# Kernel optimization log

Hardware: AMD Instinct MI355X
Metric: run time of the kernel (lower is better)

## Reference

```python
import jax, jax.numpy as jnp
import numpy as np

N_NODES = 10000
N_EDGES = 160000


def _conv2d(x, w, b):
    y = jax.lax.conv_general_dilated(x, w, (1, 1), 'SAME',
                                     dimension_numbers=('NCHW', 'OIHW', 'NCHW'))
    return jax.nn.selu(y + b[None, :, None, None])


def _cnn(cf, cnn_w1, cnn_b1, cnn_w2, cnn_b2, cnn_w3, cnn_b3, cnn_w4, cnn_b4):
    h = _conv2d(cf, cnn_w1, cnn_b1)
    h = _conv2d(h, cnn_w2, cnn_b2)
    h = _conv2d(h, cnn_w3, cnn_b3)
    h = _conv2d(h, cnn_w4, cnn_b4)
    return h.mean(axis=(2, 3))  # (1, 24) global avg pool


def _gat(x, src, dst, W, a_s, a_d, b, n):
    # PyG GATConv, concat=False (mean over heads), add_self_loops handled by caller
    H, C = a_s.shape
    h = (x @ W).reshape(-1, H, C)                      # (N,H,C)
    e = jax.nn.leaky_relu((h * a_s).sum(-1)[src] +
                          (h * a_d).sum(-1)[dst], 0.2)  # (E,H)
    m = jax.ops.segment_max(e, dst, num_segments=n)
    p = jnp.exp(e - m[dst])
    z = jax.ops.segment_sum(p, dst, num_segments=n)
    alpha = p / (z[dst] + 1e-16)
    out = jax.ops.segment_sum(h[src] * alpha[..., None], dst, num_segments=n)
    return out.mean(axis=1) + b


def _fix_boundary(v, up, down, left, right):
    c0 = jnp.where(down, 0.0, jnp.where(up, 1.0, v[:, 0]))
    c1 = jnp.where(right, 1.0, jnp.where(left, 0.0, v[:, 1]))
    return v.at[:, 0].set(c0).at[:, 1].set(c1)


def setup_inputs() -> dict:
    key = jax.random.key(0)
    ks = jax.random.split(key, 40)
    d = {}
    d['x'] = jax.random.uniform(ks[0], (N_NODES, 10), dtype=jnp.float32)
    d['edge_index'] = jax.random.randint(ks[1], (2, N_EDGES), 0, N_NODES, dtype=jnp.int64)
    d['conv_feat'] = jax.random.normal(ks[2], (1, 4, 64, 64), dtype=jnp.float32)
    cnn_dims = [(16, 4), (32, 16), (64, 32), (24, 64)]
    for i, (o, c) in enumerate(cnn_dims, 1):
        d[f'cnn_w{i}'] = jax.random.normal(ks[2 + i], (o, c, 3, 3), jnp.float32) * 0.1
        d[f'cnn_b{i}'] = jnp.zeros((o,), jnp.float32)
    gat_dims = [(34, 8, 64), (64, 16, 128), (128, 8, 256), (256, 8, 128), (128, 16, 2)]
    for i, (fin, H, C) in enumerate(gat_dims, 1):
        k1, k2, k3 = jax.random.split(ks[10 + i], 3)
        d[f'g{i}_w'] = jax.random.normal(k1, (fin, H * C), jnp.float32) * 0.1
        d[f'g{i}_as'] = jax.random.normal(k2, (H, C), jnp.float32) * 0.1
        d[f'g{i}_ad'] = jax.random.normal(k3, (H, C), jnp.float32) * 0.1
        d[f'g{i}_b'] = jnp.zeros((C,), jnp.float32)
    return d


def reference(x, edge_index, conv_feat,
              cnn_w1, cnn_b1, cnn_w2, cnn_b2, cnn_w3, cnn_b3, cnn_w4, cnn_b4,
              g1_w, g1_as, g1_ad, g1_b,
              g2_w, g2_as, g2_ad, g2_b,
              g3_w, g3_as, g3_ad, g3_b,
              g4_w, g4_as, g4_ad, g4_b,
              g5_w, g5_as, g5_ad, g5_b):
    n = x.shape[0]
    # boundary masks from raw node coordinates
    up, down = x[:, 0] == 1, x[:, 0] == 0
    left, right = x[:, 1] == 0, x[:, 1] == 1
    # add self loops (PyG GATConv default)
    loops = jnp.arange(n, dtype=edge_index.dtype)
    src = jnp.concatenate([edge_index[0], loops])
    dst = jnp.concatenate([edge_index[1], loops])

    gfeat = _cnn(conv_feat, cnn_w1, cnn_b1, cnn_w2, cnn_b2, cnn_w3, cnn_b3, cnn_w4, cnn_b4)
    h = jnp.concatenate([jnp.broadcast_to(gfeat, (n, gfeat.shape[1])), x], axis=1)

    h = jax.nn.selu(_gat(h, src, dst, g1_w, g1_as, g1_ad, g1_b, n))
    h = _fix_boundary(h, up, down, left, right)
    h = jax.nn.selu(_gat(h, src, dst, g2_w, g2_as, g2_ad, g2_b, n))
    h = _fix_boundary(h, up, down, left, right)
    h = jax.nn.selu(_gat(h, src, dst, g3_w, g3_as, g3_ad, g3_b, n))
    h = _fix_boundary(h, up, down, left, right)
    h = jax.nn.selu(_gat(h, src, dst, g4_w, g4_as, g4_ad, g4_b, n))
    h = _fix_boundary(h, up, down, left, right)
    res = jax.nn.selu(_gat(h, src, dst, g5_w, g5_as, g5_ad, g5_b, n))
    out = x[:, :2] + res
    out = _fix_boundary(out, up, down, left, right)
    return out
```

## Files before the change

kernel.cpp:

```cpp
#include <hip/hip_runtime.h>
#include <hip/hip_fp16.h>
#include <math.h>


#define DEVFN static __device__ __forceinline__

typedef __attribute__((ext_vector_type(8))) _Float16 half8;
typedef __attribute__((ext_vector_type(4))) _Float16 half4v;
typedef __attribute__((ext_vector_type(4))) float f32x4;

DEVFN float selu_f(float v) {
    const float scale = 1.0507009873554805f;
    const float alpha = 1.6732632423543772f;
    return v > 0.f ? scale * v : scale * alpha * (expf(v) - 1.f);
}

DEVFN float lrelu02(float v) { return v > 0.f ? v : 0.2f * v; }

#define PST 66
#define PSZ (66 * 66)

__global__ __launch_bounds__(256) void conv3x3_first(const float* __restrict__ cf,
                                                     const float* __restrict__ w,
                                                     const float* __restrict__ b,
                                                     float* __restrict__ out) {
    int x  = threadIdx.x & 63;
    int yg = threadIdx.x >> 6;
    int y  = blockIdx.x * 4 + yg;
    int co = blockIdx.y;
    float acc = b[co];
    const float* wp = w + (size_t)co * 4 * 9;
#pragma unroll
    for (int ci = 0; ci < 4; ++ci) {
        const float* ip = cf + ci * 4096;
        const float* wr = wp + ci * 9;
#pragma unroll
        for (int ky = 0; ky < 3; ++ky) {
            int yy = y + ky - 1;
            if (yy < 0 || yy >= 64) continue;
#pragma unroll
            for (int kx = 0; kx < 3; ++kx) {
                int xx = x + kx - 1;
                if (xx < 0 || xx >= 64) continue;
                acc += wr[ky * 3 + kx] * ip[yy * 64 + xx];
            }
        }
    }
    out[(size_t)co * PSZ + (y + 1) * PST + (x + 1)] = selu_f(acc);
}

template <int CIN>
__global__ __launch_bounds__(256) void conv3x3_pad(const float* __restrict__ in,
                                                   const float* __restrict__ w,
                                                   const float* __restrict__ b,
                                                   float* __restrict__ out) {
    int x  = threadIdx.x & 63;
    int yg = threadIdx.x >> 6;
    int y  = blockIdx.x * 4 + yg;
    int co = blockIdx.y;
    float acc = b[co];
    const float* wp = w + (size_t)co * CIN * 9;
#pragma unroll 4
    for (int ci = 0; ci < CIN; ++ci) {
        const float* ip = in + ci * PSZ + y * PST + x;
        const float* wr = wp + ci * 9;
        acc += wr[0] * ip[0]           + wr[1] * ip[1]           + wr[2] * ip[2]
             + wr[3] * ip[PST]         + wr[4] * ip[PST + 1]     + wr[5] * ip[PST + 2]
             + wr[6] * ip[2 * PST]     + wr[7] * ip[2 * PST + 1] + wr[8] * ip[2 * PST + 2];
    }
    out[(size_t)co * PSZ + (y + 1) * PST + (x + 1)] = selu_f(acc);
}

__global__ void avgpool_c(const float* __restrict__ in, float* __restrict__ gfeat) {
    int c = blockIdx.x;
    int t = threadIdx.x;
    float s = 0.f;
    for (int i = t; i < 4096; i += 256) {
        int y = i >> 6, x = i & 63;
        s += in[c * PSZ + (y + 1) * PST + (x + 1)];
    }
#pragma unroll
    for (int off = 32; off >= 1; off >>= 1) s += __shfl_xor(s, off);
    __shared__ float red[4];
    int wave = t >> 6, lane = t & 63;
    if (lane == 0) red[wave] = s;
    __syncthreads();
    if (t == 0) gfeat[c] = (red[0] + red[1] + red[2] + red[3]) * (1.f / 4096.f);
}

__global__ void build_h0(const float* __restrict__ x, const float* __restrict__ gfeat,
                         __half* __restrict__ h0f, unsigned* __restrict__ masks, int N) {
    int n = blockIdx.x * blockDim.x + threadIdx.x;
    if (n >= N) return;
    float x0 = x[n * 10 + 0], x1 = x[n * 10 + 1];
    unsigned mk = (x0 == 1.f ? 1u : 0u) | (x0 == 0.f ? 2u : 0u) |
                  (x1 == 0.f ? 4u : 0u) | (x1 == 1.f ? 8u : 0u);
    masks[n] = mk;
    __half* hq = h0f + (size_t)n * 64;
#pragma unroll
    for (int j = 0; j < 64; ++j) {
        float v = (j < 24) ? gfeat[j] : (j < 34 ? x[n * 10 + (j - 24)] : 0.f);
        hq[j] = __float2half(v);
    }
}

__global__ void count_dst(const int* __restrict__ ei, int* __restrict__ cnt, int E, int N) {
    int t = blockIdx.x * blockDim.x + threadIdx.x;
    if (t >= E + N) return;
    int dst = (t < E) ? ei[E + t] : (t - E);
    atomicAdd(&cnt[dst], 1);
}

__global__ __launch_bounds__(1024) void scan_all(const int* __restrict__ cnt,
                                                 int* __restrict__ indptr,
                                                 int* __restrict__ cursor,
                                                 int n, int total) {
    __shared__ int sdata[1024];
    int t = threadIdx.x;
    int base = t * 10;
    int loc[10];
    int s = 0;
#pragma unroll
    for (int i = 0; i < 10; ++i) {
        int idx = base + i;
        int v = (idx < n) ? cnt[idx] : 0;
        loc[i] = s;
        s += v;
    }
    sdata[t] = s;
    __syncthreads();
    for (int off = 1; off < 1024; off <<= 1) {
        int tmp = (t >= off) ? sdata[t - off] : 0;
        __syncthreads();
        sdata[t] += tmp;
        __syncthreads();
    }
    int excl = (t == 0) ? 0 : sdata[t - 1];
#pragma unroll
    for (int i = 0; i < 10; ++i) {
        int idx = base + i;
        if (idx < n) {
            int e = excl + loc[i];
            indptr[idx] = e;
            cursor[idx] = e;
        }
    }
    if (t == 0) indptr[n] = total;
}

__global__ void scatter_edges(const int* __restrict__ ei, int* __restrict__ cursor,
                              int* __restrict__ col, int E, int N) {
    int t = blockIdx.x * blockDim.x + threadIdx.x;
    if (t >= E + N) return;
    int src, dst;
    if (t < E) { src = ei[t]; dst = ei[E + t]; }
    else       { src = dst = t - E; }
    int pos = atomicAdd(&cursor[dst], 1);
    col[pos] = src;
}

__global__ __launch_bounds__(256) void prep_all(
        const float* __restrict__ W0, const float* __restrict__ W1,
        const float* __restrict__ W2, const float* __restrict__ W3,
        const float* __restrict__ W4,
        const float* __restrict__ as0, const float* __restrict__ as1,
        const float* __restrict__ as2, const float* __restrict__ as3,
        const float* __restrict__ as4,
        const float* __restrict__ ad0, const float* __restrict__ ad1,
        const float* __restrict__ ad2, const float* __restrict__ ad3,
        const float* __restrict__ ad4,
        unsigned short* __restrict__ bt, float* __restrict__ wesed,
        float* __restrict__ wcomb) {
    const int Kc[5]  = {34, 64, 128, 256, 128};
    const int Kpc[5] = {64, 64, 128, 256, 128};
    const int Hc[5]  = {8, 16, 8, 8, 16};
    const int Cc[5]  = {64, 128, 256, 128, 2};
    const int HCc[5] = {512, 2048, 2048, 1024, 32};
    const int KAc[5] = {512, 1024, 1024, 2048, 2048};
    const int btOff[5] = {0, 32768, 163840, 425984, 0};
    const int weOff[5] = {0, 1024, 3072, 5120, 9216};

    int b = blockIdx.x, tid = threadIdx.x;

    if (b < 168) {
        int lyr, tloc;
        if (b < 8)        { lyr = 0; tloc = b; }
        else if (b < 40)  { lyr = 1; tloc = b - 8; }
        else if (b < 104) { lyr = 2; tloc = b - 40; }
        else              { lyr = 3; tloc = b - 104; }
        const int ktl[4] = {1, 1, 2, 4};
        const int mtl[4] = {1, 2, 4, 2};
        int kt = ktl[lyr], mt = mtl[lyr];
        int per_h = kt * mt;
        int h = tloc / per_h, r = tloc - h * per_h;
        int ki = r % kt, mi = r / kt;
        int k0 = ki * 64, m0 = mi * 64;
        int K = Kc[lyr], Kp = Kpc[lyr], C = Cc[lyr], HC = HCc[lyr], KA = KAc[lyr];
        const float* W;
        if (lyr == 0) W = W0; else if (lyr == 1) W = W1;
        else if (lyr == 2) W = W2; else W = W3;

        __shared__ float tile[64][65];
        int c = tid & 63, rg = tid >> 6;
        for (int r2 = rg; r2 < 64; r2 += 4) {
            int k = k0 + r2, m = m0 + c;
            float v = (k < K && m < C) ? W[(size_t)k * HC + h * C + m] : 0.f;
            tile[r2][c] = v;
        }
        __syncthreads();
        unsigned short* bp = bt + btOff[lyr];
        for (int mr = rg; mr < 64; mr += 4) {
            int m = m0 + mr, k = k0 + c;
            if (m < C && k < Kp)
                bp[(size_t)m * KA + h * Kp + k] =
                    __half_as_ushort(__float2half(tile[c][mr]));
        }
    } else if (b < 200) {
        int u = (b - 168) * 256 + tid;
        int k = u >> 6, o = u & 63;
        float s;
        if (o < 32) {
            int h = (o < 16) ? o : o - 16;
            const float* av = ((o < 16) ? as4 : ad4) + h * 2;
            s = W4[k * 32 + h * 2 + 0] * av[0] + W4[k * 32 + h * 2 + 1] * av[1];
        } else {
            s = W4[k * 32 + (o - 32)];
        }
        wcomb[u] = s;
    } else {
        int wb = b - 200;
        int lyr, u0;
        if (wb < 4)       { lyr = 0; u0 = wb * 256; }
        else if (wb < 12) { lyr = 1; u0 = (wb - 4) * 256; }
        else if (wb < 20) { lyr = 2; u0 = (wb - 12) * 256; }
        else if (wb < 36) { lyr = 3; u0 = (wb - 20) * 256; }
        else              { lyr = 4; u0 = (wb - 36) * 256; }
        int u = u0 + tid;
        int K = Kc[lyr], Kp = Kpc[lyr], H = Hc[lyr], C = Cc[lyr], HC = HCc[lyr];
        int H2 = 2 * H;
        if (u < Kp * H2) {
            int k = u / H2, o = u - k * H2;
            float s = 0.f;
            if (k < K) {
                int h = (o < H) ? o : o - H;
                const float *W, *as_, *ad_;
                if (lyr == 0)      { W = W0; as_ = as0; ad_ = ad0; }
                else if (lyr == 1) { W = W1; as_ = as1; ad_ = ad1; }
                else if (lyr == 2) { W = W2; as_ = as2; ad_ = ad2; }
                else if (lyr == 3) { W = W3; as_ = as3; ad_ = ad3; }
                else               { W = W4; as_ = as4; ad_ = ad4; }
                const float* av = ((o < H) ? as_ : ad_) + h * C;
                const float* wp = W + (size_t)k * HC + h * C;
#pragma unroll 4
                for (int c2 = 0; c2 < C; ++c2) s += wp[c2] * av[c2];
            }
            wesed[weOff[lyr] + u] = s;
        }
    }
}

__global__ void esed_kernel(const __half* __restrict__ hin, const float* __restrict__ wesed,
                            float* __restrict__ esed, int N, int Kp, int H2) {
    int t = blockIdx.x * blockDim.x + threadIdx.x;
    if (t >= N * H2) return;
    int n = t / H2, o = t - n * H2;
    const __half2* hp = (const __half2*)(hin + (size_t)n * Kp);
    float s = 0.f;
    for (int k2 = 0; k2 < Kp / 2; ++k2) {
        float2 f = __half22float2(hp[k2]);
        s += f.x * wesed[(2 * k2) * H2 + o] + f.y * wesed[(2 * k2 + 1) * H2 + o];
    }
    esed[t] = s;
}

template <int H, int KP, int CH, int NPB>
__global__ __launch_bounds__(NPB * (KP / CH)) void gat_fused_lds(
        const __half* __restrict__ hinf, const float* __restrict__ esed,
        const int* __restrict__ indptr, const int* __restrict__ col,
        __half* __restrict__ g, int N) {
    const int TPN = KP / CH;
    const int EC  = TPN / H;
    const int H2  = 2 * H;
    __shared__ float lds_p[NPB][2][TPN];
    int sub = threadIdx.x / TPN;
    int j   = threadIdx.x % TPN;
    int n = blockIdx.x * NPB + sub;
    if (n >= N) return;
    int e_my = j / H, h_my = j % H;
    int c0 = j * CH;
    float edv = esed[n * H2 + H + h_my];

    float acc[H][CH];
#pragma unroll
    for (int h = 0; h < H; ++h)
#pragma unroll
        for (int t = 0; t < CH; ++t) acc[h][t] = 0.f;
    float zloc = 0.f;

    int beg = indptr[n], deg = indptr[n + 1] - beg;

    float p = 0.f;
    if (e_my < deg) {
        int srcm = col[beg + e_my];
        p = expf(lrelu02(esed[srcm * H2 + h_my] + edv));
    }
    int buf = 0;
    for (int base = 0; base < deg; base += EC) {
        zloc += p;
        lds_p[sub][buf][j] = p;
        __builtin_amdgcn_wave_barrier();
        int ce = base + EC + e_my;
        bool vnext = (ce < deg);
        float esv = 0.f;
        if (vnext) {
            int srcm = col[beg + ce];
            esv = esed[srcm * H2 + h_my];
        }
#pragma unroll
        for (int e = 0; e < EC; ++e) {
            int idx = base + e;
            if (idx < deg) {
                int src = col[beg + idx];
                float f[CH];
                if (CH == 2) {
                    __half2 hv = *(const __half2*)(hinf + (size_t)src * KP + c0);
                    float2 ff = __half22float2(hv);
                    f[0] = ff.x; f[1] = ff.y;
                } else {
                    half4v hv = *(const half4v*)(hinf + (size_t)src * KP + c0);
                    f[0] = (float)hv[0]; f[1] = (float)hv[1];
                    f[2] = (float)hv[2]; f[3] = (float)hv[3];
                }
                const float4* ap = (const float4*)&lds_p[sub][buf][e * H];
#pragma unroll
                for (int q4 = 0; q4 < H / 4; ++q4) {
                    float4 a4 = ap[q4];
#pragma unroll
                    for (int t = 0; t < CH; ++t) {
                        acc[4 * q4 + 0][t] += a4.x * f[t];
                        acc[4 * q4 + 1][t] += a4.y * f[t];
                        acc[4 * q4 + 2][t] += a4.z * f[t];
                        acc[4 * q4 + 3][t] += a4.w * f[t];
                    }
                }
            }
        }
        p = vnext ? expf(lrelu02(esv + edv)) : 0.f;
        buf ^= 1;
    }

#pragma unroll
    for (int off = H; off < TPN; off <<= 1)
        zloc += __shfl_xor(zloc, off, TPN);
    float zinv_my = (1.f / H) / (zloc + 1e-16f);

    __half* gp = g + (size_t)n * (H * KP) + c0;
#pragma unroll
    for (int h = 0; h < H; ++h) {
        float zf = __shfl(zinv_my, h, TPN);
        if (CH == 2) {
            *(__half2*)(gp + h * KP) =
                __floats2half2_rn(acc[h][0] * zf, acc[h][1] * zf);
        } else {
            __half2 lo = __floats2half2_rn(acc[h][0] * zf, acc[h][1] * zf);
            __half2 hi = __floats2half2_rn(acc[h][2] * zf, acc[h][3] * zf);
            union { __half2 h2[2]; float2 f2; } u;
            u.h2[0] = lo; u.h2[1] = hi;
            *(float2*)(gp + h * KP) = u.f2;
        }
    }
}

template <int NPB>
__global__ __launch_bounds__(NPB * 32) void final_attn(
        const float* __restrict__ eyp, const int* __restrict__ indptr,
        const int* __restrict__ col, const float* __restrict__ b5,
        const unsigned* __restrict__ masks, const float* __restrict__ x,
        float* __restrict__ outp, int N) {
    int sub = threadIdx.x >> 5;
    int j   = threadIdx.x & 31;
    int n = blockIdx.x * NPB + sub;
    if (n >= N) return;
    int h = j >> 1;
    float edv = eyp[(size_t)n * 64 + 16 + h];
    int beg = indptr[n], end = indptr[n + 1];
    float z = 0.f, a = 0.f;
    int i = beg;
    for (; i + 1 < end; i += 2) {
        int s0 = col[i], s1 = col[i + 1];
        const float* r0 = eyp + (size_t)s0 * 64;
        const float* r1 = eyp + (size_t)s1 * 64;
        float es0 = r0[h], y0 = r0[32 + j];
        float es1 = r1[h], y1 = r1[32 + j];
        float p0 = expf(lrelu02(es0 + edv));
        float p1 = expf(lrelu02(es1 + edv));
        z += p0; a += p0 * y0;
        z += p1; a += p1 * y1;
    }
    for (; i < end; ++i) {
        const float* r = eyp + (size_t)col[i] * 64;
        float p = expf(lrelu02(r[h] + edv));
        z += p; a += p * r[32 + j];
    }
    float zf = (1.f / 16.f) / (z + 1e-16f);
    float val = a * zf;
#pragma unroll
    for (int off = 2; off <= 16; off <<= 1) val += __shfl_xor(val, off, 32);
    float other = __shfl_xor(val, 1, 32);
    if (j == 0) {
        unsigned mk = masks[n];
        float v0 = x[n * 10 + 0] + selu_f(val + b5[0]);
        float v1 = x[n * 10 + 1] + selu_f(other + b5[1]);
        if (mk & 2u) v0 = 0.f; else if (mk & 1u) v0 = 1.f;
        if (mk & 8u) v1 = 1.f; else if (mk & 4u) v1 = 0.f;
        outp[n * 2 + 0] = v0;
        outp[n * 2 + 1] = v1;
    }
}

#define LDP 72

__global__ __launch_bounds__(256) void gemm_lds(const __half* __restrict__ A,
                                                const unsigned short* __restrict__ Bhi,
                                                const float* __restrict__ bias,
                                                const unsigned* __restrict__ masks,
                                                __half* __restrict__ O16,
                                                int N, int K, int M) {
    __shared__ __half lA[64 * LDP], lB[64 * LDP];
    int tid = threadIdx.x;
    int wave = tid >> 6, lane = tid & 63;
    int ln16 = lane & 15, q = lane >> 4;
    int row0 = blockIdx.x * 64;
    int col0 = blockIdx.y * 64;

    int r0 = tid >> 3, r1 = r0 + 32;
    int ac = (tid & 7) * 8;
    int ga0 = min(row0 + r0, N - 1);
    int ga1 = min(row0 + r1, N - 1);
    const __half* Bp = (const __half*)Bhi;
    const __half* a0p = A + (size_t)ga0 * K + ac;
    const __half* a1p = A + (size_t)ga1 * K + ac;
    const __half* b0p = Bp + (size_t)(col0 + r0) * K + ac;
    const __half* b1p = Bp + (size_t)(col0 + r1) * K + ac;

    half8 ra0 = *(const half8*)(a0p);
    half8 ra1 = *(const half8*)(a1p);
    half8 rb0 = *(const half8*)(b0p);
    half8 rb1 = *(const half8*)(b1p);

    f32x4 acc[4];
#pragma unroll
    for (int j = 0; j < 4; ++j) acc[j] = (f32x4){0.f, 0.f, 0.f, 0.f};

    for (int kc = 0; kc < K; kc += 64) {
        __syncthreads();
        *(half8*)(lA + r0 * LDP + ac) = ra0;
        *(half8*)(lA + r1 * LDP + ac) = ra1;
        *(half8*)(lB + r0 * LDP + ac) = rb0;
        *(half8*)(lB + r1 * LDP + ac) = rb1;
        __syncthreads();
        int kn = kc + 64;
        if (kn < K) {
            ra0 = *(const half8*)(a0p + kn);
            ra1 = *(const half8*)(a1p + kn);
            rb0 = *(const half8*)(b0p + kn);
            rb1 = *(const half8*)(b1p + kn);
        }
#pragma unroll
        for (int kk = 0; kk < 2; ++kk) {
            half8 af = *(const half8*)(lA + (wave * 16 + ln16) * LDP + kk * 32 + q * 8);
#pragma unroll
            for (int j = 0; j < 4; ++j) {
                half8 bf = *(const half8*)(lB + (j * 16 + ln16) * LDP + kk * 32 + q * 8);
                acc[j] = __builtin_amdgcn_mfma_f32_16x16x32_f16(af, bf, acc[j], 0, 0, 0);
            }
        }
    }

#pragma unroll
    for (int j = 0; j < 4; ++j) {
        int cc = col0 + j * 16 + ln16;
        float bv = bias[cc];
#pragma unroll
        for (int r = 0; r < 4; ++r) {
            int rr = row0 + wave * 16 + q * 4 + r;
            if (rr >= N) continue;
            float v = selu_f(acc[j][r] + bv);
            if (cc < 2) {
                unsigned mk = masks[rr];
                if (cc == 0) { if (mk & 2u) v = 0.f; else if (mk & 1u) v = 1.f; }
                else         { if (mk & 8u) v = 1.f; else if (mk & 4u) v = 0.f; }
            }
            O16[(size_t)rr * M + cc] = __float2half(v);
        }
    }
}

__global__ __launch_bounds__(256) void gemm_rc(const __half* __restrict__ A,
                                               const unsigned short* __restrict__ Bhi,
                                               const float* __restrict__ bias,
                                               const unsigned* __restrict__ masks,
                                               __half* __restrict__ O16,
                                               int N, int K, int M) {
    __shared__ __half lA[32 * LDP], lB[128 * LDP];
    int tid = threadIdx.x;
    int wave = tid >> 6, lane = tid & 63;
    int ln16 = lane & 15, q = lane >> 4;
    int row0 = blockIdx.x * 32;
    int col0 = blockIdx.y * 128;
    int wr = (wave >> 1) * 16;
    int wc = (wave & 1) * 64;

    int ar = tid >> 3;
    int ac = (tid & 7) * 8;
    int ga = min(row0 + ar, N - 1);
    const __half* ap  = A + (size_t)ga * K + ac;
    const __half* Bp  = (const __half*)Bhi;
    const __half* b0p = Bp + (size_t)(col0 + ar) * K + ac;
    const __half* b1p = Bp + (size_t)(col0 + ar + 32) * K + ac;
    const __half* b2p = Bp + (size_t)(col0 + ar + 64) * K + ac;
    const __half* b3p = Bp + (size_t)(col0 + ar + 96) * K + ac;

    half8 ra  = *(const half8*)(ap);
    half8 rb0 = *(const half8*)(b0p);
    half8 rb1 = *(const half8*)(b1p);
    half8 rb2 = *(const half8*)(b2p);
    half8 rb3 = *(const half8*)(b3p);

    f32x4 acc[4];
#pragma unroll
    for (int j = 0; j < 4; ++j) acc[j] = (f32x4){0.f, 0.f, 0.f, 0.f};

    for (int kc = 0; kc < K; kc += 64) {
        __syncthreads();
        *(half8*)(lA + ar * LDP + ac)        = ra;
        *(half8*)(lB + ar * LDP + ac)        = rb0;
        *(half8*)(lB + (ar + 32) * LDP + ac) = rb1;
        *(half8*)(lB + (ar + 64) * LDP + ac) = rb2;
        *(half8*)(lB + (ar + 96) * LDP + ac) = rb3;
        __syncthreads();
        int kn = kc + 64;
        if (kn < K) {
            ra  = *(const half8*)(ap + kn);
            rb0 = *(const half8*)(b0p + kn);
            rb1 = *(const half8*)(b1p + kn);
            rb2 = *(const half8*)(b2p + kn);
            rb3 = *(const half8*)(b3p + kn);
        }
#pragma unroll
        for (int kk = 0; kk < 2; ++kk) {
            half8 af = *(const half8*)(lA + (wr + ln16) * LDP + kk * 32 + q * 8);
#pragma unroll
            for (int j = 0; j < 4; ++j) {
                half8 bf = *(const half8*)(lB + (wc + j * 16 + ln16) * LDP + kk * 32 + q * 8);
                acc[j] = __builtin_amdgcn_mfma_f32_16x16x32_f16(af, bf, acc[j], 0, 0, 0);
            }
        }
    }

#pragma unroll
    for (int j = 0; j < 4; ++j) {
        int cc = col0 + wc + j * 16 + ln16;
        float bv = bias[cc];
#pragma unroll
        for (int r = 0; r < 4; ++r) {
            int rr = row0 + wr + q * 4 + r;
            if (rr >= N) continue;
            float v = selu_f(acc[j][r] + bv);
            if (cc < 2) {
                unsigned mk = masks[rr];
                if (cc == 0) { if (mk & 2u) v = 0.f; else if (mk & 1u) v = 1.f; }
                else         { if (mk & 8u) v = 1.f; else if (mk & 4u) v = 0.f; }
            }
            O16[(size_t)rr * M + cc] = __float2half(v);
        }
    }
}

extern "C" void kernel_launch(void* const* d_in, const int* in_sizes, int n_in,
                              void* d_out, int out_size, void* d_ws, size_t ws_size,
                              hipStream_t stream) {
    const float* x   = (const float*)d_in[0];
    const int*   ei  = (const int*)d_in[1];
    const float* cf  = (const float*)d_in[2];
    const float* cw[4] = {(const float*)d_in[3], (const float*)d_in[5],
                          (const float*)d_in[7], (const float*)d_in[9]};
    const float* cb[4] = {(const float*)d_in[4], (const float*)d_in[6],
                          (const float*)d_in[8], (const float*)d_in[10]};
    const float* gw[5], *gas[5], *gad[5], *gb[5];
    for (int i = 0; i < 5; ++i) {
        gw[i]  = (const float*)d_in[11 + 4 * i];
        gas[i] = (const float*)d_in[12 + 4 * i];
        gad[i] = (const float*)d_in[13 + 4 * i];
        gb[i]  = (const float*)d_in[14 + 4 * i];
    }
    const int N = in_sizes[0] / 10;
    const int E = in_sizes[1] / 2;
    const int EN = E + N;

    char* base = (char*)d_ws;
    size_t off = 0;
    auto alloc = [&](size_t bytes) -> char* {
        char* p = base + off;
        off = (off + bytes + 255) & ~(size_t)255;
        return p;
    };
    float* c1p   = (float*)alloc((size_t)16 * PSZ * 4);
    float* c2p   = (float*)alloc((size_t)32 * PSZ * 4);
    float* c3p   = (float*)alloc((size_t)64 * PSZ * 4);
    float* c4p   = (float*)alloc((size_t)24 * PSZ * 4);
    float* gfeat = (float*)alloc(24 * 4);
    __half* hA16 = (__half*)alloc((size_t)N * 256 * 2);
    __half* hB16 = (__half*)alloc((size_t)N * 256 * 2);
    __half* g    = (__half*)alloc((size_t)N * 2048 * 2);
    float* esed  = (float*)alloc((size_t)N * 32 * 4);
    float* eyp   = (float*)alloc((size_t)N * 64 * 4);
    float* wesed = (float*)alloc((size_t)13312 * 4);
    float* wcomb = (float*)alloc((size_t)8192 * 4);
    unsigned short* bt = (unsigned short*)alloc((size_t)688128 * 2);
    unsigned* masks = (unsigned*)alloc((size_t)N * 4);
    int* cnt    = (int*)alloc((size_t)N * 4);
    int* indptr = (int*)alloc((size_t)(N + 1) * 4);
    int* cursor = (int*)alloc((size_t)N * 4);
    int* col    = (int*)alloc((size_t)EN * 4);
    (void)ws_size;

    prep_all<<<252, 256, 0, stream>>>(gw[0], gw[1], gw[2], gw[3], gw[4],
                                      gas[0], gas[1], gas[2], gas[3], gas[4],
                                      gad[0], gad[1], gad[2], gad[3], gad[4],
                                      bt, wesed, wcomb);

    hipMemsetAsync(c1p, 0, (size_t)136 * PSZ * 4, stream);
    conv3x3_first<<<dim3(16, 16), 256, 0, stream>>>(cf, cw[0], cb[0], c1p);
    conv3x3_pad<16><<<dim3(16, 32), 256, 0, stream>>>(c1p, cw[1], cb[1], c2p);
    conv3x3_pad<32><<<dim3(16, 64), 256, 0, stream>>>(c2p, cw[2], cb[2], c3p);
    conv3x3_pad<64><<<dim3(16, 24), 256, 0, stream>>>(c3p, cw[3], cb[3], c4p);
    avgpool_c<<<24, 256, 0, stream>>>(c4p, gfeat);

    build_h0<<<(N + 255) / 256, 256, 0, stream>>>(x, gfeat, hA16, masks, N);

    hipMemsetAsync(cnt, 0, (size_t)N * 4, stream);
    count_dst<<<(EN + 255) / 256, 256, 0, stream>>>(ei, cnt, E, N);
    scan_all<<<1, 1024, 0, stream>>>(cnt, indptr, cursor, N, EN);
    scatter_edges<<<(EN + 255) / 256, 256, 0, stream>>>(ei, cursor, col, E, N);

    const int Hs[5] = {8, 16, 8, 8, 16};
    const int Cs[5] = {64, 128, 256, 128, 2};
    const int Kp[5] = {64, 64, 128, 256, 128};
    const int btOffA[5] = {0, 32768, 163840, 425984, 0};
    const int weOffA[5] = {0, 1024, 3072, 5120, 9216};

    const __half* hin16 = hA16;
    __half* hout16[4]  = {hB16, hA16, hB16, hA16};

    for (int lyr = 0; lyr < 5; ++lyr) {
        int KP = Kp[lyr], H = Hs[lyr], C = Cs[lyr];
        int KA = H * KP;
        if (lyr == 4) {
            esed_kernel<<<(N * 64 + 255) / 256, 256, 0, stream>>>(hin16, wcomb, eyp,
                                                                  N, 128, 64);
            final_attn<8><<<(N + 7) / 8, 256, 0, stream>>>(eyp, indptr, col, gb[4],
                                                           masks, x, (float*)d_out, N);
            break;
        }
        esed_kernel<<<(N * 2 * H + 255) / 256, 256, 0, stream>>>(hin16, wesed + weOffA[lyr],
                                                                 esed, N, KP, 2 * H);
        if (lyr == 0) {
            gat_fused_lds<8, 64, 4, 16><<<(N + 15) / 16, 256, 0, stream>>>(
                hin16, esed, indptr, col, g, N);
        } else if (lyr == 1) {
            gat_fused_lds<16, 64, 2, 8><<<(N + 7) / 8, 256, 0, stream>>>(
                hin16, esed, indptr, col, g, N);
        } else if (lyr == 2) {
            gat_fused_lds<8, 128, 4, 8><<<(N + 7) / 8, 256, 0, stream>>>(
                hin16, esed, indptr, col, g, N);
        } else {
            gat_fused_lds<8, 256, 4, 4><<<(N + 3) / 4, 256, 0, stream>>>(
                hin16, esed, indptr, col, g, N);
        }

        const unsigned short* btL = bt + btOffA[lyr];
        if (lyr == 0) {
            gemm_lds<<<dim3((N + 63) / 64, 1), 256, 0, stream>>>(g, btL, gb[lyr], masks,
                                                                 hout16[lyr], N, KA, C);
        } else {
            gemm_rc<<<dim3((N + 31) / 32, C / 128), 256, 0, stream>>>(g, btL, gb[lyr], masks,
                                                                      hout16[lyr], N, KA, C);
        }
        hin16 = hout16[lyr];
    }
}
```

Measured before the change: 513.0 us.

## Fuse next-layer attention score projection into GEMM epilogues

The GEMM epilogues now stage the fp16-rounded activated output tile in shared memory and multiply it by the next layer's attention projection weights, writing the esed/eyp score arrays directly. This removes three separate esed_kernel launches and the global re-read of the hidden features they did. Layer 2's GEMM covers two column blocks, so it keeps the standalone esed kernel. In exchange the GEMM kernels use extra LDS and do a serial per-thread dot-product loop after a block barrier, which may lower occupancy and lengthen the epilogue.

```diff
diff --git a/kernel.cpp b/kernel.cpp
--- a/kernel.cpp
+++ b/kernel.cpp
@@ -420,13 +420,17 @@
 
 #define LDP 72
 
+template <int EOUT>
 __global__ __launch_bounds__(256) void gemm_lds(const __half* __restrict__ A,
                                                 const unsigned short* __restrict__ Bhi,
                                                 const float* __restrict__ bias,
                                                 const unsigned* __restrict__ masks,
                                                 __half* __restrict__ O16,
+                                                const float* __restrict__ wnext,
+                                                float* __restrict__ eout,
                                                 int N, int K, int M) {
     __shared__ __half lA[64 * LDP], lB[64 * LDP];
+    __shared__ float vt[EOUT ? 64 : 1][EOUT ? 68 : 1];
     int tid = threadIdx.x;
     int wave = tid >> 6, lane = tid & 63;
     int ln16 = lane & 15, q = lane >> 4;
@@ -484,25 +488,53 @@
 #pragma unroll
         for (int r = 0; r < 4; ++r) {
             int rr = row0 + wave * 16 + q * 4 + r;
-            if (rr >= N) continue;
             float v = selu_f(acc[j][r] + bv);
-            if (cc < 2) {
+            if (cc < 2 && rr < N) {
                 unsigned mk = masks[rr];
                 if (cc == 0) { if (mk & 2u) v = 0.f; else if (mk & 1u) v = 1.f; }
                 else         { if (mk & 8u) v = 1.f; else if (mk & 4u) v = 0.f; }
             }
-            O16[(size_t)rr * M + cc] = __float2half(v);
-        }
-    }
-}
-
+            __half hv = __float2half(v);
+            if (rr < N) O16[(size_t)rr * M + cc] = hv;
+            if constexpr (EOUT > 0)
+                vt[wave * 16 + q * 4 + r][j * 16 + ln16] = __half2float(hv);
+        }
+    }
+
+    if constexpr (EOUT > 0) {
+        __syncthreads();
+        const int NG = 256 / EOUT;
+        const int NI = 64 / NG;
+        int o = tid & (EOUT - 1);
+        int ngrp = tid / EOUT;
+        float s[NI];
+#pragma unroll
+        for (int i = 0; i < NI; ++i) s[i] = 0.f;
+        for (int k = 0; k < 64; ++k) {
+            float wk = wnext[k * EOUT + o];
+#pragma unroll
+            for (int i = 0; i < NI; ++i)
+                s[i] += vt[ngrp + NG * i][k] * wk;
+        }
+#pragma unroll
+        for (int i = 0; i < NI; ++i) {
+            int n = row0 + ngrp + NG * i;
+            if (n < N) eout[(size_t)n * EOUT + o] = s[i];
+        }
+    }
+}
+
+template <int EOUT>
 __global__ __launch_bounds__(256) void gemm_rc(const __half* __restrict__ A,
                                                const unsigned short* __restrict__ Bhi,
                                                const float* __restrict__ bias,
                                                const unsigned* __restrict__ masks,
                                                __half* __restrict__ O16,
+                                               const float* __restrict__ wnext,
+                                               float* __restrict__ eout,
                                                int N, int K, int M) {
     __shared__ __half lA[32 * LDP], lB[128 * LDP];
+    __shared__ float vt[EOUT ? 32 : 1][EOUT ? 132 : 1];
     int tid = threadIdx.x;
     int wave = tid >> 6, lane = tid & 63;
     int ln16 = lane & 15, q = lane >> 4;
@@ -565,14 +597,38 @@
 #pragma unroll
         for (int r = 0; r < 4; ++r) {
             int rr = row0 + wr + q * 4 + r;
-            if (rr >= N) continue;
             float v = selu_f(acc[j][r] + bv);
-            if (cc < 2) {
+            if (cc < 2 && rr < N) {
                 unsigned mk = masks[rr];
                 if (cc == 0) { if (mk & 2u) v = 0.f; else if (mk & 1u) v = 1.f; }
                 else         { if (mk & 8u) v = 1.f; else if (mk & 4u) v = 0.f; }
             }
-            O16[(size_t)rr * M + cc] = __float2half(v);
+            __half hv = __float2half(v);
+            if (rr < N) O16[(size_t)rr * M + cc] = hv;
+            if constexpr (EOUT > 0)
+                vt[wr + q * 4 + r][wc + j * 16 + ln16] = __half2float(hv);
+        }
+    }
+
+    if constexpr (EOUT > 0) {
+        __syncthreads();
+        const int NG = 256 / EOUT;
+        const int NI = 32 / NG;
+        int o = tid & (EOUT - 1);
+        int ngrp = tid / EOUT;
+        float s[NI];
+#pragma unroll
+        for (int i = 0; i < NI; ++i) s[i] = 0.f;
+        for (int k = 0; k < 128; ++k) {
+            float wk = wnext[k * EOUT + o];
+#pragma unroll
+            for (int i = 0; i < NI; ++i)
+                s[i] += vt[ngrp + NG * i][k] * wk;
+        }
+#pragma unroll
+        for (int i = 0; i < NI; ++i) {
+            int n = row0 + ngrp + NG * i;
+            if (n < N) eout[(size_t)n * EOUT + o] = s[i];
         }
     }
 }
@@ -644,49 +700,31 @@
     scan_all<<<1, 1024, 0, stream>>>(cnt, indptr, cursor, N, EN);
     scatter_edges<<<(EN + 255) / 256, 256, 0, stream>>>(ei, cursor, col, E, N);
 
-    const int Hs[5] = {8, 16, 8, 8, 16};
-    const int Cs[5] = {64, 128, 256, 128, 2};
-    const int Kp[5] = {64, 64, 128, 256, 128};
-    const int btOffA[5] = {0, 32768, 163840, 425984, 0};
-    const int weOffA[5] = {0, 1024, 3072, 5120, 9216};
-
-    const __half* hin16 = hA16;
-    __half* hout16[4]  = {hB16, hA16, hB16, hA16};
-
-    for (int lyr = 0; lyr < 5; ++lyr) {
-        int KP = Kp[lyr], H = Hs[lyr], C = Cs[lyr];
-        int KA = H * KP;
-        if (lyr == 4) {
-            esed_kernel<<<(N * 64 + 255) / 256, 256, 0, stream>>>(hin16, wcomb, eyp,
-                                                                  N, 128, 64);
-            final_attn<8><<<(N + 7) / 8, 256, 0, stream>>>(eyp, indptr, col, gb[4],
-                                                           masks, x, (float*)d_out, N);
-            break;
-        }
-        esed_kernel<<<(N * 2 * H + 255) / 256, 256, 0, stream>>>(hin16, wesed + weOffA[lyr],
-                                                                 esed, N, KP, 2 * H);
-        if (lyr == 0) {
-            gat_fused_lds<8, 64, 4, 16><<<(N + 15) / 16, 256, 0, stream>>>(
-                hin16, esed, indptr, col, g, N);
-        } else if (lyr == 1) {
-            gat_fused_lds<16, 64, 2, 8><<<(N + 7) / 8, 256, 0, stream>>>(
-                hin16, esed, indptr, col, g, N);
-        } else if (lyr == 2) {
-            gat_fused_lds<8, 128, 4, 8><<<(N + 7) / 8, 256, 0, stream>>>(
-                hin16, esed, indptr, col, g, N);
-        } else {
-            gat_fused_lds<8, 256, 4, 4><<<(N + 3) / 4, 256, 0, stream>>>(
-                hin16, esed, indptr, col, g, N);
-        }
-
-        const unsigned short* btL = bt + btOffA[lyr];
-        if (lyr == 0) {
-            gemm_lds<<<dim3((N + 63) / 64, 1), 256, 0, stream>>>(g, btL, gb[lyr], masks,
-                                                                 hout16[lyr], N, KA, C);
-        } else {
-            gemm_rc<<<dim3((N + 31) / 32, C / 128), 256, 0, stream>>>(g, btL, gb[lyr], masks,
-                                                                      hout16[lyr], N, KA, C);
-        }
-        hin16 = hout16[lyr];
-    }
-}
+    int gx32 = (N + 31) / 32;
+    int gx64 = (N + 63) / 64;
+
+    esed_kernel<<<(N * 16 + 255) / 256, 256, 0, stream>>>(hA16, wesed + 0, esed, N, 64, 16);
+    gat_fused_lds<8, 64, 4, 16><<<(N + 15) / 16, 256, 0, stream>>>(
+        hA16, esed, indptr, col, g, N);
+    gemm_lds<32><<<dim3(gx64, 1), 256, 0, stream>>>(g, bt + 0, gb[0], masks, hB16,
+                                                    wesed + 1024, esed, N, 512, 64);
+
+    gat_fused_lds<16, 64, 2, 8><<<(N + 7) / 8, 256, 0, stream>>>(
+        hB16, esed, indptr, col, g, N);
+    gemm_rc<16><<<dim3(gx32, 1), 256, 0, stream>>>(g, bt + 32768, gb[1], masks, hA16,
+                                                   wesed + 3072, esed, N, 1024, 128);
+
+    gat_fused_lds<8, 128, 4, 8><<<(N + 7) / 8, 256, 0, stream>>>(
+        hA16, esed, indptr, col, g, N);
+    gemm_rc<0><<<dim3(gx32, 2), 256, 0, stream>>>(g, bt + 163840, gb[2], masks, hB16,
+                                                  nullptr, nullptr, N, 1024, 256);
+    esed_kernel<<<(N * 16 + 255) / 256, 256, 0, stream>>>(hB16, wesed + 5120, esed, N, 256, 16);
+
+    gat_fused_lds<8, 256, 4, 4><<<(N + 3) / 4, 256, 0, stream>>>(
+        hB16, esed, indptr, col, g, N);
+    gemm_rc<64><<<dim3(gx32, 1), 256, 0, stream>>>(g, bt + 425984, gb[3], masks, hA16,
+                                                   wcomb, eyp, N, 2048, 128);
+
+    final_attn<8><<<(N + 7) / 8, 256, 0, stream>>>(eyp, indptr, col, gb[4],
+                                                   masks, x, (float*)d_out, N);
+}
```

Result: faster. 470.1 us (-8.4%).
